# Kernel tuning notes

Hardware: AMD Instinct MI355X
Metric: run time of the kernel (lower is better)

The kernel has to match this reference:

```python
import jax, jax.numpy as jnp
import numpy as np

R = 8          # shuffle_rate
HEADS = 4
DIM_HEAD = 64


def setup_inputs() -> dict:
    key = jax.random.key(0)
    k1, k2, k3 = jax.random.split(key, 3)
    dim = 64
    C = dim * R * R            # 4096, token channel dim after unshuffle
    inner = HEADS * DIM_HEAD   # 256
    x = jax.random.normal(k1, (8, dim, 256, 256), dtype=jnp.float32)
    W_qkv = jax.random.normal(k2, (C, 3 * inner), dtype=jnp.float32) * (C ** -0.5)
    W_out = jax.random.normal(k3, (inner, C), dtype=jnp.float32) * (inner ** -0.5)
    b_out = jnp.zeros((C,), dtype=jnp.float32)
    return {"x": x, "W_qkv": W_qkv, "W_out": W_out, "b_out": b_out}


def reference(x, W_qkv, W_out, b_out):
    scale = DIM_HEAD ** -0.5
    B, C0, H0, W0 = x.shape
    h, w = H0 // R, W0 // R
    N = h * w
    C = C0 * R * R
    # PixelUnshuffle: [B,C0,H0,W0] -> [B, C0*R*R, h, w]
    xd = x.reshape(B, C0, h, R, w, R).transpose(0, 1, 3, 5, 2, 4).reshape(B, C, h, w)
    # flatten spatial -> tokens [B, N, C]
    tokens = xd.reshape(B, C, N).transpose(0, 2, 1)
    qkv = tokens @ W_qkv                                   # [B, N, 3*inner]
    q, k, v = jnp.split(qkv, 3, axis=-1)
    def heads(t):  # [B,N,inner] -> [B,H,N,d]
        return t.reshape(B, N, HEADS, DIM_HEAD).transpose(0, 2, 1, 3)
    q, k, v = heads(q), heads(k), heads(v)
    dots = jnp.einsum('bhnd,bhmd->bhnm', q, k) * scale
    attn = jax.nn.softmax(dots, axis=-1)
    out = jnp.einsum('bhnm,bhmd->bhnd', attn, v)
    out = out.transpose(0, 2, 1, 3).reshape(B, N, HEADS * DIM_HEAD)
    y = out @ W_out + b_out                                # [B, N, C]
    y = y.transpose(0, 2, 1).reshape(B, C, h, w)
    # PixelShuffle: [B, C0*R*R, h, w] -> [B, C0, H0, W0]
    y = y.reshape(B, C0, R, R, h, w).transpose(0, 1, 4, 2, 5, 3).reshape(B, C0, H0, W0)
    return y
```

## Files before the change

### kernel.cpp

```cpp
#include <hip/hip_runtime.h>

typedef unsigned short u16;
typedef __attribute__((ext_vector_type(8))) short s16x8;
typedef __attribute__((ext_vector_type(4))) short s16x4;
typedef __attribute__((ext_vector_type(4))) float f32x4;

__device__ __forceinline__ u16 f2bf(float f) {
    unsigned int u;
    __builtin_memcpy(&u, &f, 4);
    unsigned int r = u + 0x7FFFu + ((u >> 16) & 1u);
    return (u16)(r >> 16);
}

__device__ __forceinline__ void gl_lds16(const u16* g, u16* l) {
    __builtin_amdgcn_global_load_lds(
        (const __attribute__((address_space(1))) unsigned int*)g,
        (__attribute__((address_space(3))) unsigned int*)l,
        16, 0, 0);
}

__global__ __launch_bounds__(256) void k_transpose(const float* __restrict__ in,
                                                   u16* __restrict__ out,
                                                   int rows, int cols) {
    __shared__ float tile[64][65];
    int bx = blockIdx.x * 64, by = blockIdx.y * 64;
    int tx = threadIdx.x & 63, ty = threadIdx.x >> 6;
    for (int i = ty; i < 64; i += 4)
        tile[i][tx] = in[(size_t)(by + i) * cols + bx + tx];
    __syncthreads();
    for (int i = ty; i < 64; i += 4)
        out[(size_t)(bx + i) * rows + by + tx] = f2bf(tile[tx][i]);
}

__global__ __launch_bounds__(256) void k_gemm_qkv(const float* __restrict__ x,
                                                  const u16* __restrict__ Bt,
                                                  u16* __restrict__ Qo,
                                                  u16* __restrict__ Ko,
                                                  u16* __restrict__ Vo) {
    const int K = 4096;
    __shared__ u16 As[128 * 64];
    __shared__ u16 Bs[128 * 64];
    const int tid = threadIdx.x;
    const int wave = tid >> 6, lane = tid & 63;
    const int quad = lane >> 4, l15 = lane & 15;
    const int wm = wave >> 1, wn = wave & 1;
    const int tm = blockIdx.y * 128, tn = blockIdx.x * 128;

    f32x4 acc[4][4] = {};

    for (int k0 = 0; k0 < K; k0 += 64) {
        __syncthreads();
        for (int t = 0; t < 4; ++t) {
            int s = t * 256 + tid;
            int m = tm + (s >> 3);
            int c = k0 + (s & 7) * 8;
            int b = m >> 10, n = m & 1023, yy = n >> 5, xx = n & 31;
            int c0 = c >> 6, r1 = (c >> 3) & 7;
            const float* src = x + ((size_t)((b * 64 + c0) * 256 + yy * 8 + r1)) * 256 + xx * 8;
            float4 f0 = *(const float4*)(src);
            float4 f1 = *(const float4*)(src + 4);
            s16x8 v;
            v[0] = (short)f2bf(f0.x); v[1] = (short)f2bf(f0.y);
            v[2] = (short)f2bf(f0.z); v[3] = (short)f2bf(f0.w);
            v[4] = (short)f2bf(f1.x); v[5] = (short)f2bf(f1.y);
            v[6] = (short)f2bf(f1.z); v[7] = (short)f2bf(f1.w);
            *(s16x8*)(As + s * 8) = v;
        }
        for (int t = 0; t < 4; ++t) {
            int c = wave * 256 + t * 64 + lane;
            int row = c >> 3, kc = c & 7;
            gl_lds16(Bt + (size_t)(tn + row) * K + k0 + kc * 8,
                     Bs + (wave * 256 + t * 64) * 8);
        }
        __syncthreads();
        for (int kk = 0; kk < 64; kk += 32) {
            s16x8 af[4], bf[4];
            for (int i = 0; i < 4; ++i)
                af[i] = *(const s16x8*)(As + (wm * 64 + i * 16 + l15) * 64 + kk + quad * 8);
            for (int j = 0; j < 4; ++j)
                bf[j] = *(const s16x8*)(Bs + (wn * 64 + j * 16 + l15) * 64 + kk + quad * 8);
            for (int i = 0; i < 4; ++i)
                for (int j = 0; j < 4; ++j)
                    acc[i][j] = __builtin_amdgcn_mfma_f32_16x16x32_bf16(af[i], bf[j], acc[i][j], 0, 0, 0);
        }
    }

    for (int i = 0; i < 4; ++i) {
        int mb = tm + wm * 64 + i * 16 + quad * 4;
        for (int j = 0; j < 4; ++j) {
            int col = tn + wn * 64 + j * 16 + l15;
            int which = col >> 8, h = (col >> 6) & 3, d = col & 63;
            u16* dst = (which == 0) ? Qo : (which == 1) ? Ko : Vo;
            for (int r = 0; r < 4; ++r) {
                int m = mb + r;
                int b = m >> 10, n = m & 1023;
                dst[((size_t)((b * 4 + h) * 1024 + n)) * 64 + d] = f2bf(acc[i][j][r]);
            }
        }
    }
}

__global__ __launch_bounds__(256) void k_attn(const u16* __restrict__ Qb,
                                              const u16* __restrict__ Kb,
                                              const u16* __restrict__ Vb,
                                              u16* __restrict__ aout) {
    const int bh = blockIdx.y;
    const int q0 = blockIdx.x * 64;
    const int tid = threadIdx.x;
    const int wave = tid >> 6, lane = tid & 63;
    const int quad = lane >> 4, l15 = lane & 15;
    const size_t base = (size_t)bh * 1024 * 64;
    const float scale = 0.125f;

    __shared__ u16 Ks[64 * 64];
    __shared__ u16 Vts[64 * 68];
    __shared__ u16 Ps[4][16 * 64];

    s16x8 aq0, aq1;
    {
        const u16* qp = Qb + base + (size_t)(q0 + wave * 16 + l15) * 64 + quad * 8;
        aq0 = *(const s16x8*)(qp);
        aq1 = *(const s16x8*)(qp + 32);
    }

    float m_i[4], l_i[4];
    f32x4 o[4] = {};
    for (int r = 0; r < 4; ++r) { m_i[r] = -1e30f; l_i[r] = 0.f; }

    for (int t = 0; t < 16; ++t) {
        __syncthreads();
        for (int e = 0; e < 2; ++e) {
            int s = e * 256 + tid;
            int row = s >> 3, off = (s & 7) * 8;
            *(s16x8*)(Ks + row * 64 + off) =
                *(const s16x8*)(Kb + base + (size_t)(t * 64 + row) * 64 + off);
        }
        for (int e = 0; e < 16; ++e) {
            int s = e * 256 + tid;
            int kv = s >> 6, d = s & 63;
            Vts[d * 68 + kv] = Vb[base + (size_t)(t * 64 + kv) * 64 + d];
        }
        __syncthreads();

        f32x4 s4[4];
        for (int j = 0; j < 4; ++j) {
            const u16* kr = Ks + (j * 16 + l15) * 64 + quad * 8;
            s16x8 b0 = *(const s16x8*)(kr);
            s16x8 b1 = *(const s16x8*)(kr + 32);
            f32x4 c = {};
            c = __builtin_amdgcn_mfma_f32_16x16x32_bf16(aq0, b0, c, 0, 0, 0);
            c = __builtin_amdgcn_mfma_f32_16x16x32_bf16(aq1, b1, c, 0, 0, 0);
            s4[j] = c;
        }

        for (int r = 0; r < 4; ++r) {
            float sv0 = s4[0][r] * scale, sv1 = s4[1][r] * scale;
            float sv2 = s4[2][r] * scale, sv3 = s4[3][r] * scale;
            float mt = fmaxf(fmaxf(sv0, sv1), fmaxf(sv2, sv3));
            for (int off = 1; off < 16; off <<= 1)
                mt = fmaxf(mt, __shfl_xor(mt, off, 64));
            float mn = fmaxf(m_i[r], mt);
            float alpha = __expf(m_i[r] - mn);
            m_i[r] = mn;
            float p0 = __expf(sv0 - mn), p1 = __expf(sv1 - mn);
            float p2 = __expf(sv2 - mn), p3 = __expf(sv3 - mn);
            u16* pw = Ps[wave] + (quad * 4 + r) * 64 + l15;
            pw[0]  = f2bf(p0);
            pw[16] = f2bf(p1);
            pw[32] = f2bf(p2);
            pw[48] = f2bf(p3);
            float rs = p0 + p1 + p2 + p3;
            for (int off = 1; off < 16; off <<= 1)
                rs += __shfl_xor(rs, off, 64);
            l_i[r] = l_i[r] * alpha + rs;
            for (int dt = 0; dt < 4; ++dt) o[dt][r] *= alpha;
        }

        for (int kk = 0; kk < 64; kk += 32) {
            s16x8 pf = *(const s16x8*)(Ps[wave] + l15 * 64 + kk + quad * 8);
            for (int dt = 0; dt < 4; ++dt) {
                const u16* vr = Vts + (dt * 16 + l15) * 68 + kk + quad * 8;
                s16x4 v0 = *(const s16x4*)(vr);
                s16x4 v1 = *(const s16x4*)(vr + 4);
                s16x8 vf;
                vf[0] = v0[0]; vf[1] = v0[1]; vf[2] = v0[2]; vf[3] = v0[3];
                vf[4] = v1[0]; vf[5] = v1[1]; vf[6] = v1[2]; vf[7] = v1[3];
                o[dt] = __builtin_amdgcn_mfma_f32_16x16x32_bf16(pf, vf, o[dt], 0, 0, 0);
            }
        }
    }

    int b = bh >> 2, h = bh & 3;
    for (int dt = 0; dt < 4; ++dt)
        for (int r = 0; r < 4; ++r) {
            int qrow = q0 + wave * 16 + quad * 4 + r;
            float val = o[dt][r] / l_i[r];
            aout[((size_t)(b) * 1024 + qrow) * 256 + h * 64 + dt * 16 + l15] = f2bf(val);
        }
}

__global__ __launch_bounds__(256) void k_gemm_out(const u16* __restrict__ A,
                                                  const u16* __restrict__ Bt,
                                                  const float* __restrict__ bias,
                                                  float* __restrict__ out) {
    const int K = 256;
    __shared__ u16 As[128 * 64];
    __shared__ u16 Bs[128 * 64];
    const int tid = threadIdx.x;
    const int wave = tid >> 6, lane = tid & 63;
    const int quad = lane >> 4, l15 = lane & 15;
    const int wm = wave >> 1, wn = wave & 1;
    const int tm = blockIdx.y * 128, tn = blockIdx.x * 128;

    f32x4 acc[4][4] = {};

    for (int k0 = 0; k0 < K; k0 += 64) {
        __syncthreads();
        for (int t = 0; t < 4; ++t) {
            int c = wave * 256 + t * 64 + lane;
            int row = c >> 3, kc = c & 7;
            gl_lds16(A + (size_t)(tm + row) * K + k0 + kc * 8,
                     As + (wave * 256 + t * 64) * 8);
        }
        for (int t = 0; t < 4; ++t) {
            int c = wave * 256 + t * 64 + lane;
            int row = c >> 3, kc = c & 7;
            gl_lds16(Bt + (size_t)(tn + row) * K + k0 + kc * 8,
                     Bs + (wave * 256 + t * 64) * 8);
        }
        __syncthreads();
        for (int kk = 0; kk < 64; kk += 32) {
            s16x8 af[4], bf[4];
            for (int i = 0; i < 4; ++i)
                af[i] = *(const s16x8*)(As + (wm * 64 + i * 16 + l15) * 64 + kk + quad * 8);
            for (int j = 0; j < 4; ++j)
                bf[j] = *(const s16x8*)(Bs + (wn * 64 + j * 16 + l15) * 64 + kk + quad * 8);
            for (int i = 0; i < 4; ++i)
                for (int j = 0; j < 4; ++j)
                    acc[i][j] = __builtin_amdgcn_mfma_f32_16x16x32_bf16(af[i], bf[j], acc[i][j], 0, 0, 0);
        }
    }

    for (int i = 0; i < 4; ++i) {
        int mb = tm + wm * 64 + i * 16 + quad * 4;
        for (int j = 0; j < 4; ++j) {
            int col = tn + wn * 64 + j * 16 + l15;
            float bb = bias[col];
            int c0 = col >> 6, r1 = (col >> 3) & 7, r2 = col & 7;
            for (int r = 0; r < 4; ++r) {
                int m = mb + r;
                int b = m >> 10, n = m & 1023, yy = n >> 5, xx = n & 31;
                size_t oidx = ((size_t)((b * 64 + c0) * 256 + yy * 8 + r1)) * 256 + xx * 8 + r2;
                out[oidx] = acc[i][j][r] + bb;
            }
        }
    }
}

extern "C" void kernel_launch(void* const* d_in, const int* in_sizes, int n_in,
                              void* d_out, int out_size, void* d_ws, size_t ws_size,
                              hipStream_t stream) {
    (void)in_sizes; (void)n_in; (void)out_size; (void)ws_size;
    const float* x    = (const float*)d_in[0];
    const float* Wqkv = (const float*)d_in[1];
    const float* Wout = (const float*)d_in[2];
    const float* bout = (const float*)d_in[3];
    float* out = (float*)d_out;

    u16* ws    = (u16*)d_ws;
    u16* wqkvT = ws;
    u16* woutT = wqkvT + 3145728;
    u16* Qb    = woutT + 1048576;
    u16* Kb    = Qb + 2097152;
    u16* Vb    = Kb + 2097152;
    u16* aoutb = Vb + 2097152;

    k_transpose<<<dim3(12, 64), 256, 0, stream>>>(Wqkv, wqkvT, 4096, 768);
    k_transpose<<<dim3(64, 4), 256, 0, stream>>>(Wout, woutT, 256, 4096);
    k_gemm_qkv<<<dim3(6, 64), 256, 0, stream>>>(x, wqkvT, Qb, Kb, Vb);
    k_attn<<<dim3(16, 32), 256, 0, stream>>>(Qb, Kb, Vb, aoutb);
    k_gemm_out<<<dim3(32, 64), 256, 0, stream>>>(aoutb, woutT, bout, out);
}
```

Measured before the change: 445.6 us.

## Pre-unshuffle tokens to bf16 and split-K the QKV GEMM with a reduce pass

```diff
diff --git a/kernel.cpp b/kernel.cpp
--- a/kernel.cpp
+++ b/kernel.cpp
@@ -17,6 +17,30 @@
         (const __attribute__((address_space(1))) unsigned int*)g,
         (__attribute__((address_space(3))) unsigned int*)l,
         16, 0, 0);
+}
+
+__global__ __launch_bounds__(256) void k_unshuffle(const float* __restrict__ x,
+                                                   u16* __restrict__ tok) {
+    int idx = blockIdx.x * 256 + threadIdx.x;
+    int r1  = idx & 7;
+    int xxg = (idx >> 3) & 7;
+    int yy  = (idx >> 6) & 31;
+    int c0  = (idx >> 11) & 63;
+    int b   = idx >> 17;
+
+    const float* src = x + ((size_t)((b * 64 + c0) * 256 + yy * 8 + r1)) * 256 + xxg * 32;
+    int mbase = b * 1024 + yy * 32 + xxg * 4;
+    int cbase = c0 * 64 + r1 * 8;
+    for (int q = 0; q < 4; ++q) {
+        float4 f0 = *(const float4*)(src + q * 8);
+        float4 f1 = *(const float4*)(src + q * 8 + 4);
+        s16x8 v;
+        v[0] = (short)f2bf(f0.x); v[1] = (short)f2bf(f0.y);
+        v[2] = (short)f2bf(f0.z); v[3] = (short)f2bf(f0.w);
+        v[4] = (short)f2bf(f1.x); v[5] = (short)f2bf(f1.y);
+        v[6] = (short)f2bf(f1.z); v[7] = (short)f2bf(f1.w);
+        *(s16x8*)(tok + (size_t)(mbase + q) * 4096 + cbase) = v;
+    }
 }
 
 __global__ __launch_bounds__(256) void k_transpose(const float* __restrict__ in,
@@ -32,11 +56,9 @@
         out[(size_t)(bx + i) * rows + by + tx] = f2bf(tile[tx][i]);
 }
 
-__global__ __launch_bounds__(256) void k_gemm_qkv(const float* __restrict__ x,
+__global__ __launch_bounds__(256) void k_gemm_qkv(const u16* __restrict__ A,
                                                   const u16* __restrict__ Bt,
-                                                  u16* __restrict__ Qo,
-                                                  u16* __restrict__ Ko,
-                                                  u16* __restrict__ Vo) {
+                                                  float* __restrict__ P) {
     const int K = 4096;
     __shared__ u16 As[128 * 64];
     __shared__ u16 Bs[128 * 64];
@@ -45,26 +67,17 @@
     const int quad = lane >> 4, l15 = lane & 15;
     const int wm = wave >> 1, wn = wave & 1;
     const int tm = blockIdx.y * 128, tn = blockIdx.x * 128;
+    const int z = blockIdx.z;
 
     f32x4 acc[4][4] = {};
 
-    for (int k0 = 0; k0 < K; k0 += 64) {
+    for (int k0 = z * 2048; k0 < (z + 1) * 2048; k0 += 64) {
         __syncthreads();
         for (int t = 0; t < 4; ++t) {
-            int s = t * 256 + tid;
-            int m = tm + (s >> 3);
-            int c = k0 + (s & 7) * 8;
-            int b = m >> 10, n = m & 1023, yy = n >> 5, xx = n & 31;
-            int c0 = c >> 6, r1 = (c >> 3) & 7;
-            const float* src = x + ((size_t)((b * 64 + c0) * 256 + yy * 8 + r1)) * 256 + xx * 8;
-            float4 f0 = *(const float4*)(src);
-            float4 f1 = *(const float4*)(src + 4);
-            s16x8 v;
-            v[0] = (short)f2bf(f0.x); v[1] = (short)f2bf(f0.y);
-            v[2] = (short)f2bf(f0.z); v[3] = (short)f2bf(f0.w);
-            v[4] = (short)f2bf(f1.x); v[5] = (short)f2bf(f1.y);
-            v[6] = (short)f2bf(f1.z); v[7] = (short)f2bf(f1.w);
-            *(s16x8*)(As + s * 8) = v;
+            int c = wave * 256 + t * 64 + lane;
+            int row = c >> 3, kc = c & 7;
+            gl_lds16(A + (size_t)(tm + row) * K + k0 + kc * 8,
+                     As + (wave * 256 + t * 64) * 8);
         }
         for (int t = 0; t < 4; ++t) {
             int c = wave * 256 + t * 64 + lane;
@@ -85,19 +98,28 @@
         }
     }
 
+    float* Pz = P + (size_t)z * 8192 * 768;
     for (int i = 0; i < 4; ++i) {
         int mb = tm + wm * 64 + i * 16 + quad * 4;
         for (int j = 0; j < 4; ++j) {
             int col = tn + wn * 64 + j * 16 + l15;
-            int which = col >> 8, h = (col >> 6) & 3, d = col & 63;
-            u16* dst = (which == 0) ? Qo : (which == 1) ? Ko : Vo;
-            for (int r = 0; r < 4; ++r) {
-                int m = mb + r;
-                int b = m >> 10, n = m & 1023;
-                dst[((size_t)((b * 4 + h) * 1024 + n)) * 64 + d] = f2bf(acc[i][j][r]);
-            }
-        }
-    }
+            for (int r = 0; r < 4; ++r)
+                Pz[(size_t)(mb + r) * 768 + col] = acc[i][j][r];
+        }
+    }
+}
+
+__global__ __launch_bounds__(256) void k_qkv_reduce(const float* __restrict__ P,
+                                                    u16* __restrict__ Qo,
+                                                    u16* __restrict__ Ko,
+                                                    u16* __restrict__ Vo) {
+    int col = blockIdx.x * 256 + threadIdx.x;
+    int m   = blockIdx.y;
+    float v = P[(size_t)m * 768 + col] + P[(size_t)(8192 * 768) + (size_t)m * 768 + col];
+    int which = col >> 8, h = (col >> 6) & 3, d = col & 63;
+    int b = m >> 10, n = m & 1023;
+    u16* dst = (which == 0) ? Qo : (which == 1) ? Ko : Vo;
+    dst[((size_t)((b * 4 + h) * 1024 + n)) * 64 + d] = f2bf(v);
 }
 
 __global__ __launch_bounds__(256) void k_attn(const u16* __restrict__ Qb,
@@ -267,17 +289,21 @@
     const float* bout = (const float*)d_in[3];
     float* out = (float*)d_out;
 
-    u16* ws    = (u16*)d_ws;
-    u16* wqkvT = ws;
-    u16* woutT = wqkvT + 3145728;
-    u16* Qb    = woutT + 1048576;
-    u16* Kb    = Qb + 2097152;
-    u16* Vb    = Kb + 2097152;
-    u16* aoutb = Vb + 2097152;
-
+    u16* ws     = (u16*)d_ws;
+    u16* tokens = ws;
+    u16* wqkvT  = tokens + 33554432;
+    u16* woutT  = wqkvT + 3145728;
+    u16* Qb     = woutT + 1048576;
+    u16* Kb     = Qb + 2097152;
+    u16* Vb     = Kb + 2097152;
+    u16* aoutb  = Vb + 2097152;
+    float* Pp   = (float*)(aoutb + 2097152);
+
+    k_unshuffle<<<4096, 256, 0, stream>>>(x, tokens);
     k_transpose<<<dim3(12, 64), 256, 0, stream>>>(Wqkv, wqkvT, 4096, 768);
     k_transpose<<<dim3(64, 4), 256, 0, stream>>>(Wout, woutT, 256, 4096);
-    k_gemm_qkv<<<dim3(6, 64), 256, 0, stream>>>(x, wqkvT, Qb, Kb, Vb);
+    k_gemm_qkv<<<dim3(6, 64, 2), 256, 0, stream>>>(tokens, wqkvT, Pp);
+    k_qkv_reduce<<<dim3(3, 8192), 256, 0, stream>>>(Pp, Qb, Kb, Vb);
     k_attn<<<dim3(16, 32), 256, 0, stream>>>(Qb, Kb, Vb, aoutb);
     k_gemm_out<<<dim3(32, 64), 256, 0, stream>>>(aoutb, woutT, bout, out);
 }
```

Result: faster. 428.5 us (-3.8%).
